# Performance work log

Measured on AMD Instinct MI355X. Metric: run time of the kernel, lower is better.

The kernel has to match this reference:

```python
import jax, jax.numpy as jnp
import numpy as np

N_NODES = 100000
N_EDGES = 20000
N_PAIRS = 640000
IN_CH = 128
HEADS = 4
OUT_CH = 32


def setup_inputs() -> dict:
    key = jax.random.key(0)
    k1, k2, k3, k4, k5 = jax.random.split(key, 5)
    X = jax.random.normal(k1, (N_NODES, IN_CH), dtype=jnp.float32)
    # nn.Linear(in, H*C, bias=False); stored as [in, H*C] so X0 = X @ W
    W = jax.random.normal(k2, (IN_CH, HEADS * OUT_CH), dtype=jnp.float32) * (1.0 / np.sqrt(IN_CH))
    stdv = (6.0 / (HEADS + OUT_CH)) ** 0.5
    att_e = jax.random.uniform(k3, (1, HEADS, OUT_CH), dtype=jnp.float32, minval=-stdv, maxval=stdv)
    vertex = jax.random.randint(k4, (N_PAIRS,), 0, N_NODES, dtype=jnp.int64)
    edges = jax.random.randint(k5, (N_PAIRS,), 0, N_EDGES, dtype=jnp.int64)
    return {"X": X, "W": W, "att_e": att_e, "vertex": vertex, "edges": edges}


def reference(X, W, att_e, vertex, edges):
    N = X.shape[0]
    H, C = HEADS, OUT_CH
    X0 = X @ W                                  # [N, H*C]
    Xv_hc = X0.reshape(N, H, C)
    Xve = Xv_hc[vertex]                          # [M, H, C] gather
    # scatter-mean over hyperedges
    esum = jax.ops.segment_sum(Xve, edges, num_segments=N_EDGES)
    ecnt = jax.ops.segment_sum(jnp.ones((Xve.shape[0],), X.dtype), edges, num_segments=N_EDGES)
    Xe = esum / jnp.maximum(ecnt, 1.0)[:, None, None]   # [E, H, C]
    alpha_e = (Xe * att_e).sum(-1)               # [E, H]
    a_ev = alpha_e[edges]                        # [M, H]
    alpha = jax.nn.leaky_relu(a_ev, 0.01)
    # per-vertex softmax over incident hyperedges
    amax = jax.ops.segment_max(alpha, vertex, num_segments=N)
    alpha = jnp.exp(alpha - amax[vertex])
    asum = jax.ops.segment_sum(alpha, vertex, num_segments=N)
    alpha = alpha / (asum[vertex] + 1e-8)
    Xev = Xe[edges] * alpha[:, :, None]          # [M, H, C]
    Xv = jax.ops.segment_sum(Xev, vertex, num_segments=N)
    return Xv.reshape(N, H * C) + X0
```

## Files before the change

### kernel.cpp

```cpp
#include <hip/hip_runtime.h>
#include <hip/hip_bf16.h>

#define N_NODES 100000
#define N_EDGES 20000
#define N_PAIRS 640000
#define CH 128
#define HEADS 4
#define MAXDV 32

#define NG_GEMM 1563
#define NCHUNK 125
#define ECHUNK 5120
#define EW 5120
#define VWR 6250
#define NRANGE 4
#define VBIN_R 25000

#define OFF_X0H   0UL
#define OFF_XEH   25600000UL
#define OFF_LRE   30720000UL
#define OFF_LRV   31360000UL
#define OFF_BLKE  32000000UL
#define OFF_BLKV  34560000UL
#define OFF_GSE   47060000UL
#define OFF_GSV   47162400UL
#define OFF_WT    47662400UL
#define OFF_ALPHA 47695168UL
#define OFF_OFFE  48015168UL
#define OFF_ENDE  48097088UL
#define OFF_OFFV  48179008UL
#define OFF_ENDV  48579008UL
#define OFF_PIDXE 48979008UL
#define OFF_PIDXV 51539008UL
#define OFF_CNTE  54099008UL
#define OFF_CNTV  54180928UL
#define OFF_TOT   54580928UL
#define ZERO_BYTES 8UL

typedef __attribute__((ext_vector_type(8))) short bf16x8;
typedef __attribute__((ext_vector_type(4))) float f32x4;

__device__ inline short f2bf(float f) {
    __hip_bfloat16 h = __float2bfloat16(f);
    return reinterpret_cast<short&>(h);
}
__device__ inline float bf2f(short s) {
    unsigned int u = ((unsigned int)(unsigned short)s) << 16;
    union { unsigned int u; float f; } c; c.u = u;
    return c.f;
}

__global__ __launch_bounds__(256) void k_wprep(const float* __restrict__ W,
                                               short* __restrict__ Wt) {
    const int idx = blockIdx.x * 256 + threadIdx.x;
    const int n = idx >> 7, k = idx & 127;
    Wt[n * CH + k] = f2bf(W[k * CH + n]);
}

__device__ inline void gemm_body(int gb, const float* __restrict__ X,
                                 const short* __restrict__ Wt,
                                 short* __restrict__ X0h) {
    const int t = threadIdx.x;
    const int wave = t >> 6, lane = t & 63;
    const int r0 = gb * 64 + (wave >> 1) * 32;
    const int c0 = (wave & 1) * 64;
    const int lrow = lane & 15, lk8 = (lane >> 4) * 8;

    f32x4 acc[2][4] = {};

#pragma unroll
    for (int kk = 0; kk < 4; ++kk) {
        const int ks = kk * 32 + lk8;
        bf16x8 a[2], b[4];
#pragma unroll
        for (int m = 0; m < 2; ++m) {
            int row = r0 + m * 16 + lrow;
            row = min(row, N_NODES - 1);
            const float* p = &X[(size_t)row * CH + ks];
            const float4 x0 = *(const float4*)p;
            const float4 x1 = *(const float4*)(p + 4);
            a[m][0] = f2bf(x0.x); a[m][1] = f2bf(x0.y);
            a[m][2] = f2bf(x0.z); a[m][3] = f2bf(x0.w);
            a[m][4] = f2bf(x1.x); a[m][5] = f2bf(x1.y);
            a[m][6] = f2bf(x1.z); a[m][7] = f2bf(x1.w);
        }
#pragma unroll
        for (int n = 0; n < 4; ++n) {
            int col = c0 + n * 16 + lrow;
            b[n] = *(const bf16x8*)&Wt[col * CH + ks];
        }
#pragma unroll
        for (int m = 0; m < 2; ++m)
#pragma unroll
            for (int n = 0; n < 4; ++n)
                acc[m][n] = __builtin_amdgcn_mfma_f32_16x16x32_bf16(a[m], b[n], acc[m][n], 0, 0, 0);
    }

#pragma unroll
    for (int m = 0; m < 2; ++m) {
#pragma unroll
        for (int reg = 0; reg < 4; ++reg) {
            const int row = r0 + m * 16 + (lane >> 4) * 4 + reg;
            if (row < N_NODES) {
#pragma unroll
                for (int n = 0; n < 4; ++n)
                    X0h[(size_t)row * CH + c0 + n * 16 + (lane & 15)] = f2bf(acc[m][n][reg]);
            }
        }
    }
}

__global__ __launch_bounds__(256) void k_phase1(const float* __restrict__ X,
                                                const short* __restrict__ Wt,
                                                short* __restrict__ X0h,
                                                const int* __restrict__ vertex,
                                                const int* __restrict__ edges,
                                                unsigned char* __restrict__ lrank_e,
                                                unsigned char* __restrict__ lrank_v,
                                                unsigned int* __restrict__ blkcnt_e,
                                                unsigned int* __restrict__ blkcnt_v) {
    __shared__ unsigned int hist[VWR];
    const int bid = blockIdx.x;
    const int t = threadIdx.x;

    if (bid < NRANGE * NCHUNK) {
        const int r = bid & 3, c = bid >> 2;
        for (int i = t; i < VWR; i += 256) hist[i] = 0;
        __syncthreads();
        const int base = c * ECHUNK;
        const int vmin = r * VBIN_R;
#pragma unroll
        for (int it = 0; it < 20; ++it) {
            const int m = base + it * 256 + t;
            const int loc = vertex[m] - vmin;
            if ((unsigned)loc < (unsigned)VBIN_R) {
                const unsigned sh = (unsigned)(loc & 3) * 8u;
                unsigned old = atomicAdd(&hist[loc >> 2], 1u << sh);
                lrank_v[m] = (unsigned char)((old >> sh) & 0xffu);
            }
        }
        __syncthreads();
        unsigned int* dst = &blkcnt_v[(size_t)(r * NCHUNK + c) * VWR];
        for (int w = t; w < VWR; w += 256) dst[w] = hist[w];
        return;
    }
    if (bid < NRANGE * NCHUNK + NCHUNK) {
        const int c = bid - NRANGE * NCHUNK;
        for (int i = t; i < EW; i += 256) hist[i] = 0;
        __syncthreads();
        const int base = c * ECHUNK;
#pragma unroll
        for (int it = 0; it < 20; ++it) {
            const int m = base + it * 256 + t;
            const int e = edges[m];
            const unsigned sh = (unsigned)(e & 3) * 8u;
            unsigned old = atomicAdd(&hist[e >> 2], 1u << sh);
            lrank_e[m] = (unsigned char)((old >> sh) & 0xffu);
        }
        __syncthreads();
        unsigned int* dst = &blkcnt_e[(size_t)c * EW];
        for (int w = t; w < EW; w += 256) dst[w] = hist[w];
        return;
    }
    gemm_body(bid - (NRANGE * NCHUNK + NCHUNK), X, Wt, X0h);
}

__global__ __launch_bounds__(256) void k_scan_p1(const unsigned int* __restrict__ blkcnt_e,
                                                 const unsigned int* __restrict__ blkcnt_v,
                                                 unsigned int* __restrict__ gse,
                                                 unsigned int* __restrict__ gsv) {
    const int bid = blockIdx.x;
    if (bid < 100) {
        const int gid = bid * 256 + threadIdx.x;
        const int g = gid / EW, w = gid % EW;
        unsigned s = 0;
#pragma unroll 5
        for (int i = 0; i < 25; ++i) s += blkcnt_e[(size_t)(g * 25 + i) * EW + w];
        gse[g * EW + w] = s;
        return;
    }
    const int vid = (bid - 100) * 256 + threadIdx.x;
    if (vid >= 20 * VWR) return;
    const int g = vid / VWR, w = vid % VWR;
    const int r = g / 5, cg = g % 5;
    unsigned s = 0;
#pragma unroll 5
    for (int i = 0; i < 25; ++i)
        s += blkcnt_v[(size_t)(r * NCHUNK + cg * 25 + i) * VWR + w];
    gsv[g * VWR + w] = s;
}

__global__ __launch_bounds__(256) void k_scan_p2(unsigned int* __restrict__ gse,
                                                 unsigned int* __restrict__ gsv,
                                                 int* __restrict__ cnt_e,
                                                 int* __restrict__ cnt_v) {
    const int bid = blockIdx.x;
    if (bid < 20) {
        const int w = bid * 256 + threadIdx.x;
        unsigned run = 0;
#pragma unroll
        for (int g = 0; g < 5; ++g) {
            unsigned c = gse[g * EW + w];
            gse[g * EW + w] = run;
            run += c;
        }
        int4 o = { (int)(run & 0xffu), (int)((run >> 8) & 0xffu),
                   (int)((run >> 16) & 0xffu), (int)(run >> 24) };
        *(int4*)&cnt_e[4 * w] = o;
        return;
    }
    const int id = (bid - 20) * 256 + threadIdx.x;
    if (id >= NRANGE * VWR) return;
    const int r = id / VWR, w = id % VWR;
    unsigned run = 0;
#pragma unroll
    for (int g = r * 5; g < r * 5 + 5; ++g) {
        unsigned c = gsv[g * VWR + w];
        gsv[g * VWR + w] = run;
        run += c;
    }
    int4 o = { (int)(run & 0xffu), (int)((run >> 8) & 0xffu),
               (int)((run >> 16) & 0xffu), (int)(run >> 24) };
    *(int4*)&cnt_v[r * VBIN_R + 4 * w] = o;
}

__global__ __launch_bounds__(256) void k_scan_p3(unsigned int* __restrict__ blkcnt_e,
                                                 unsigned int* __restrict__ blkcnt_v,
                                                 const unsigned int* __restrict__ gse,
                                                 const unsigned int* __restrict__ gsv) {
    const int bid = blockIdx.x;
    if (bid < 100) {
        const int gid = bid * 256 + threadIdx.x;
        const int g = gid / EW, w = gid % EW;
        unsigned run = gse[g * EW + w];
#pragma unroll 5
        for (int i = 0; i < 25; ++i) {
            const size_t idx = (size_t)(g * 25 + i) * EW + w;
            unsigned c = blkcnt_e[idx];
            blkcnt_e[idx] = run;
            run += c;
        }
        return;
    }
    const int vid = (bid - 100) * 256 + threadIdx.x;
    if (vid >= 20 * VWR) return;
    const int g = vid / VWR, w = vid % VWR;
    const int r = g / 5, cg = g % 5;
    unsigned run = gsv[g * VWR + w];
#pragma unroll 5
    for (int i = 0; i < 25; ++i) {
        const size_t idx = (size_t)(r * NCHUNK + cg * 25 + i) * VWR + w;
        unsigned c = blkcnt_v[idx];
        blkcnt_v[idx] = run;
        run += c;
    }
}

__global__ __launch_bounds__(256) void k_offsets2(const int* __restrict__ cnt_e,
                                                  int* __restrict__ off_e,
                                                  int* __restrict__ end_e,
                                                  const int* __restrict__ cnt_v,
                                                  int* __restrict__ off_v,
                                                  int* __restrict__ end_v,
                                                  int* __restrict__ totals) {
    __shared__ int s[256];
    __shared__ int base;
    const int bid = blockIdx.x, t = threadIdx.x;
    const int* cnt; int* off; int* end; int* total; int n, i;
    if (bid < 79) { cnt = cnt_e; off = off_e; end = end_e; total = &totals[0]; n = N_EDGES;  i = bid * 256 + t; }
    else          { cnt = cnt_v; off = off_v; end = end_v; total = &totals[1]; n = N_NODES; i = (bid - 79) * 256 + t; }
    const int c = (i < n) ? cnt[i] : 0;
    s[t] = c;
    __syncthreads();
    for (int d = 1; d < 256; d <<= 1) {
        int x = (t >= d) ? s[t - d] : 0;
        __syncthreads();
        s[t] += x;
        __syncthreads();
    }
    if (t == 0) base = atomicAdd(total, s[255]);
    __syncthreads();
    if (i < n) {
        int o = base + s[t] - c;
        off[i] = o;
        end[i] = o + c;
    }
}

__global__ __launch_bounds__(256) void k_scatter(const int* __restrict__ vertex,
                                                 const int* __restrict__ edges,
                                                 const unsigned char* __restrict__ lrank_e,
                                                 const unsigned char* __restrict__ lrank_v,
                                                 const unsigned int* __restrict__ blkcnt_e,
                                                 const unsigned int* __restrict__ blkcnt_v,
                                                 const int* __restrict__ off_e,
                                                 const int* __restrict__ off_v,
                                                 int* __restrict__ vlist_e,
                                                 int* __restrict__ elist_v) {
    const int m = blockIdx.x * 256 + threadIdx.x;
    const int e = edges[m];
    const int v = vertex[m];
    const int c = m / ECHUNK;
    const unsigned pe = blkcnt_e[(size_t)c * EW + (e >> 2)];
    const int er = (int)((pe >> ((unsigned)(e & 3) * 8u)) & 0xffu) + (int)lrank_e[m];
    const int r = v / VBIN_R, loc = v - r * VBIN_R;
    const unsigned pv = blkcnt_v[(size_t)(r * NCHUNK + c) * VWR + (loc >> 2)];
    const int vr = (int)((pv >> ((unsigned)(loc & 3) * 8u)) & 0xffu) + (int)lrank_v[m];
    vlist_e[off_e[e] + er] = v;
    elist_v[off_v[v] + vr] = e;
}

__global__ __launch_bounds__(256) void k_edge(const short* __restrict__ X0h,
                                              const int* __restrict__ off_e,
                                              const int* __restrict__ end_e,
                                              const int* __restrict__ vlist,
                                              const float* __restrict__ att,
                                              short* __restrict__ Xeh,
                                              float* __restrict__ alpha_le) {
    const int t = threadIdx.x;
    const int slot = t >> 5, lane = t & 31, h = lane >> 3;
    const int e = blockIdx.x * 8 + slot;
    const int s = off_e[e], en = end_e[e];
    const int deg = en - s;

    float4 acc = make_float4(0.f, 0.f, 0.f, 0.f);
    for (int c0 = 0; c0 < deg; c0 += 32) {
        const int cn = min(32, deg - c0);
        int vl = (lane < cn) ? vlist[s + c0 + lane] : 0;
#pragma unroll 4
        for (int j = 0; j < cn; ++j) {
            int vj = __shfl(vl, j, 32);
            short4 x = *(const short4*)&X0h[(size_t)vj * CH + (lane << 2)];
            acc.x += bf2f(x.x); acc.y += bf2f(x.y);
            acc.z += bf2f(x.z); acc.w += bf2f(x.w);
        }
    }
    const float invd = 1.0f / fmaxf((float)deg, 1.0f);
    float4 xe = make_float4(acc.x * invd, acc.y * invd, acc.z * invd, acc.w * invd);
    short4 xh;
    xh.x = f2bf(xe.x); xh.y = f2bf(xe.y); xh.z = f2bf(xe.z); xh.w = f2bf(xe.w);
    *(short4*)&Xeh[(size_t)e * CH + (lane << 2)] = xh;

    const float4 av = *(const float4*)&att[lane << 2];
    float p = xe.x * av.x + xe.y * av.y + xe.z * av.z + xe.w * av.w;
#pragma unroll
    for (int o = 4; o; o >>= 1) p += __shfl_xor(p, o);
    if ((lane & 7) == 0) {
        float a = p;
        alpha_le[e * HEADS + h] = (a > 0.f) ? a : 0.01f * a;
    }
}

__global__ __launch_bounds__(256) void k_vertex(const short* __restrict__ X0h,
                                                const short* __restrict__ Xeh,
                                                const float* __restrict__ alpha_le,
                                                const int* __restrict__ off_v,
                                                const int* __restrict__ end_v,
                                                const int* __restrict__ elist,
                                                float* __restrict__ out) {
    const int t = threadIdx.x;
    const int slot = t >> 5, lane = t & 31, h = lane >> 3;
    const int v = blockIdx.x * 8 + slot;
    const int s = off_v[v], en = end_v[v];
    const int deg = en - s;

    __shared__ int   se[8][MAXDV];
    __shared__ float sa[8][MAXDV * HEADS];

    if (deg <= MAXDV && lane < deg) {
        int e = elist[s + lane];
        se[slot][lane] = e;
        *(float4*)&sa[slot][lane << 2] = *(const float4*)&alpha_le[e * HEADS];
    }
    const short4 resh = *(const short4*)&X0h[(size_t)v * CH + (lane << 2)];
    __syncthreads();

    float4 acc = make_float4(0.f, 0.f, 0.f, 0.f);
    if (deg <= MAXDV) {
        float mx = -INFINITY;
        for (int j = 0; j < deg; ++j) mx = fmaxf(mx, sa[slot][(j << 2) + h]);
        float ssum = 0.f;
        for (int j = 0; j < deg; ++j) ssum += __expf(sa[slot][(j << 2) + h] - mx);
        const float inv = 1.0f / (ssum + 1e-8f);
        for (int j = 0; j < deg; ++j) {
            float w = __expf(sa[slot][(j << 2) + h] - mx) * inv;
            short4 x = *(const short4*)&Xeh[(size_t)se[slot][j] * CH + (lane << 2)];
            acc.x += w * bf2f(x.x); acc.y += w * bf2f(x.y);
            acc.z += w * bf2f(x.z); acc.w += w * bf2f(x.w);
        }
    } else {
        float mx = -INFINITY;
        for (int j = 0; j < deg; ++j) mx = fmaxf(mx, alpha_le[elist[s + j] * HEADS + h]);
        float ssum = 0.f;
        for (int j = 0; j < deg; ++j) ssum += __expf(alpha_le[elist[s + j] * HEADS + h] - mx);
        const float inv = 1.0f / (ssum + 1e-8f);
        for (int j = 0; j < deg; ++j) {
            int e = elist[s + j];
            float w = __expf(alpha_le[e * HEADS + h] - mx) * inv;
            short4 x = *(const short4*)&Xeh[(size_t)e * CH + (lane << 2)];
            acc.x += w * bf2f(x.x); acc.y += w * bf2f(x.y);
            acc.z += w * bf2f(x.z); acc.w += w * bf2f(x.w);
        }
    }
    float4 o = make_float4(acc.x + bf2f(resh.x), acc.y + bf2f(resh.y),
                           acc.z + bf2f(resh.z), acc.w + bf2f(resh.w));
    ((float4*)out)[(size_t)v * 32 + lane] = o;
}

extern "C" void kernel_launch(void* const* d_in, const int* in_sizes, int n_in,
                              void* d_out, int out_size, void* d_ws, size_t ws_size,
                              hipStream_t stream) {
    const float* X      = (const float*)d_in[0];
    const float* W      = (const float*)d_in[1];
    const float* att    = (const float*)d_in[2];
    const int*   vertex = (const int*)d_in[3];
    const int*   edges  = (const int*)d_in[4];
    float* out = (float*)d_out;

    char* ws = (char*)d_ws;
    short* X0h      = (short*)(ws + OFF_X0H);
    short* Xeh      = (short*)(ws + OFF_XEH);
    unsigned char* lrank_e = (unsigned char*)(ws + OFF_LRE);
    unsigned char* lrank_v = (unsigned char*)(ws + OFF_LRV);
    unsigned int*  blkcnt_e = (unsigned int*)(ws + OFF_BLKE);
    unsigned int*  blkcnt_v = (unsigned int*)(ws + OFF_BLKV);
    unsigned int*  gse      = (unsigned int*)(ws + OFF_GSE);
    unsigned int*  gsv      = (unsigned int*)(ws + OFF_GSV);
    short* Wt       = (short*)(ws + OFF_WT);
    float* alpha_le = (float*)(ws + OFF_ALPHA);
    int* off_e   = (int*)(ws + OFF_OFFE);
    int* end_e   = (int*)(ws + OFF_ENDE);
    int* off_v   = (int*)(ws + OFF_OFFV);
    int* end_v   = (int*)(ws + OFF_ENDV);
    int* vlist_e = (int*)(ws + OFF_PIDXE);
    int* elist_v = (int*)(ws + OFF_PIDXV);
    int* cnt_e   = (int*)(ws + OFF_CNTE);
    int* cnt_v   = (int*)(ws + OFF_CNTV);
    int* totals  = (int*)(ws + OFF_TOT);

    hipMemsetAsync(ws + OFF_TOT, 0, ZERO_BYTES, stream);

    k_wprep<<<64, 256, 0, stream>>>(W, Wt);
    k_phase1<<<NRANGE * NCHUNK + NCHUNK + NG_GEMM, 256, 0, stream>>>(
        X, Wt, X0h, vertex, edges, lrank_e, lrank_v, blkcnt_e, blkcnt_v);
    k_scan_p1<<<100 + 489, 256, 0, stream>>>(blkcnt_e, blkcnt_v, gse, gsv);
    k_scan_p2<<<20 + 98, 256, 0, stream>>>(gse, gsv, cnt_e, cnt_v);
    k_scan_p3<<<100 + 489, 256, 0, stream>>>(blkcnt_e, blkcnt_v, gse, gsv);
    k_offsets2<<<79 + 391, 256, 0, stream>>>(cnt_e, off_e, end_e, cnt_v, off_v, end_v, totals);
    k_scatter<<<N_PAIRS / 256, 256, 0, stream>>>(vertex, edges, lrank_e, lrank_v,
                                                 blkcnt_e, blkcnt_v, off_e, off_v,
                                                 vlist_e, elist_v);
    k_edge<<<N_EDGES / 8, 256, 0, stream>>>(X0h, off_e, end_e, vlist_e, att, Xeh, alpha_le);
    k_vertex<<<N_NODES / 8, 256, 0, stream>>>(X0h, Xeh, alpha_le, off_v, end_v, elist_v, out);
}
```

Measured before the change: 166.5 us.

## Widen gather loads to 16 bytes and prefetch GEMM operands one k-step ahead

The edge and vertex gather kernels now split each 32-lane group into two halves. Each half handles alternate incident rows with 16-byte bf16x8 loads instead of 8-byte short4 loads, and the partial sums are combined with a cross-half shuffle. This doubles the bytes per load and the number of rows in flight per group. The GEMM body is also software-pipelined: the X and W fragments for the next k-step are loaded while the MFMAs of the current step run, which costs extra registers. The vertex kernel's high-degree fallback leaves half the lanes idle, and output stores now come from half the lanes with two float4 writes each.

```diff
diff --git a/kernel.cpp b/kernel.cpp
--- a/kernel.cpp
+++ b/kernel.cpp
@@ -65,35 +65,49 @@
     const int r0 = gb * 64 + (wave >> 1) * 32;
     const int c0 = (wave & 1) * 64;
     const int lrow = lane & 15, lk8 = (lane >> 4) * 8;
+    const int row0 = min(r0 + lrow, N_NODES - 1);
+    const int row1 = min(r0 + 16 + lrow, N_NODES - 1);
+    const float* px0 = &X[(size_t)row0 * CH + lk8];
+    const float* px1 = &X[(size_t)row1 * CH + lk8];
+    const short* pw0 = &Wt[(size_t)(c0 + lrow) * CH + lk8];
 
     f32x4 acc[2][4] = {};
 
+    float4 xa[2][2]; bf16x8 bb[4];
+    xa[0][0] = *(const float4*)(px0); xa[0][1] = *(const float4*)(px0 + 4);
+    xa[1][0] = *(const float4*)(px1); xa[1][1] = *(const float4*)(px1 + 4);
+#pragma unroll
+    for (int n = 0; n < 4; ++n) bb[n] = *(const bf16x8*)(pw0 + n * 16 * CH);
+
 #pragma unroll
     for (int kk = 0; kk < 4; ++kk) {
-        const int ks = kk * 32 + lk8;
-        bf16x8 a[2], b[4];
+        float4 xn[2][2]; bf16x8 bn[4];
+        if (kk < 3) {
+            const int ks = (kk + 1) * 32;
+            xn[0][0] = *(const float4*)(px0 + ks); xn[0][1] = *(const float4*)(px0 + ks + 4);
+            xn[1][0] = *(const float4*)(px1 + ks); xn[1][1] = *(const float4*)(px1 + ks + 4);
+#pragma unroll
+            for (int n = 0; n < 4; ++n) bn[n] = *(const bf16x8*)(pw0 + n * 16 * CH + ks);
+        }
+        bf16x8 a[2];
 #pragma unroll
         for (int m = 0; m < 2; ++m) {
-            int row = r0 + m * 16 + lrow;
-            row = min(row, N_NODES - 1);
-            const float* p = &X[(size_t)row * CH + ks];
-            const float4 x0 = *(const float4*)p;
-            const float4 x1 = *(const float4*)(p + 4);
-            a[m][0] = f2bf(x0.x); a[m][1] = f2bf(x0.y);
-            a[m][2] = f2bf(x0.z); a[m][3] = f2bf(x0.w);
-            a[m][4] = f2bf(x1.x); a[m][5] = f2bf(x1.y);
-            a[m][6] = f2bf(x1.z); a[m][7] = f2bf(x1.w);
-        }
-#pragma unroll
-        for (int n = 0; n < 4; ++n) {
-            int col = c0 + n * 16 + lrow;
-            b[n] = *(const bf16x8*)&Wt[col * CH + ks];
+            a[m][0] = f2bf(xa[m][0].x); a[m][1] = f2bf(xa[m][0].y);
+            a[m][2] = f2bf(xa[m][0].z); a[m][3] = f2bf(xa[m][0].w);
+            a[m][4] = f2bf(xa[m][1].x); a[m][5] = f2bf(xa[m][1].y);
+            a[m][6] = f2bf(xa[m][1].z); a[m][7] = f2bf(xa[m][1].w);
         }
 #pragma unroll
         for (int m = 0; m < 2; ++m)
 #pragma unroll
             for (int n = 0; n < 4; ++n)
-                acc[m][n] = __builtin_amdgcn_mfma_f32_16x16x32_bf16(a[m], b[n], acc[m][n], 0, 0, 0);
+                acc[m][n] = __builtin_amdgcn_mfma_f32_16x16x32_bf16(a[m], bb[n], acc[m][n], 0, 0, 0);
+        if (kk < 3) {
+#pragma unroll
+            for (int m = 0; m < 2; ++m) { xa[m][0] = xn[m][0]; xa[m][1] = xn[m][1]; }
+#pragma unroll
+            for (int n = 0; n < 4; ++n) bb[n] = bn[n];
+        }
     }
 
 #pragma unroll
@@ -318,36 +332,45 @@
                                               short* __restrict__ Xeh,
                                               float* __restrict__ alpha_le) {
     const int t = threadIdx.x;
-    const int slot = t >> 5, lane = t & 31, h = lane >> 3;
+    const int slot = t >> 5, lane = t & 31;
+    const int half = lane >> 4, cl = lane & 15;
     const int e = blockIdx.x * 8 + slot;
     const int s = off_e[e], en = end_e[e];
     const int deg = en - s;
 
-    float4 acc = make_float4(0.f, 0.f, 0.f, 0.f);
+    float va[8] = {0.f, 0.f, 0.f, 0.f, 0.f, 0.f, 0.f, 0.f};
     for (int c0 = 0; c0 < deg; c0 += 32) {
         const int cn = min(32, deg - c0);
         int vl = (lane < cn) ? vlist[s + c0 + lane] : 0;
 #pragma unroll 4
-        for (int j = 0; j < cn; ++j) {
-            int vj = __shfl(vl, j, 32);
-            short4 x = *(const short4*)&X0h[(size_t)vj * CH + (lane << 2)];
-            acc.x += bf2f(x.x); acc.y += bf2f(x.y);
-            acc.z += bf2f(x.z); acc.w += bf2f(x.w);
-        }
-    }
+        for (int j = 0; j < cn; j += 2) {
+            const int jj = j + half;
+            const int vj = __shfl(vl, jj, 32);
+            if (jj < cn) {
+                bf16x8 x = *(const bf16x8*)&X0h[(size_t)vj * CH + cl * 8];
+#pragma unroll
+                for (int i = 0; i < 8; ++i) va[i] += bf2f(x[i]);
+            }
+        }
+    }
+#pragma unroll
+    for (int i = 0; i < 8; ++i) va[i] += __shfl_xor(va[i], 16);
+
     const float invd = 1.0f / fmaxf((float)deg, 1.0f);
-    float4 xe = make_float4(acc.x * invd, acc.y * invd, acc.z * invd, acc.w * invd);
-    short4 xh;
-    xh.x = f2bf(xe.x); xh.y = f2bf(xe.y); xh.z = f2bf(xe.z); xh.w = f2bf(xe.w);
-    *(short4*)&Xeh[(size_t)e * CH + (lane << 2)] = xh;
-
-    const float4 av = *(const float4*)&att[lane << 2];
-    float p = xe.x * av.x + xe.y * av.y + xe.z * av.z + xe.w * av.w;
-#pragma unroll
-    for (int o = 4; o; o >>= 1) p += __shfl_xor(p, o);
-    if ((lane & 7) == 0) {
-        float a = p;
-        alpha_le[e * HEADS + h] = (a > 0.f) ? a : 0.01f * a;
+    bf16x8 xh;
+    float xe[8];
+#pragma unroll
+    for (int i = 0; i < 8; ++i) { xe[i] = va[i] * invd; xh[i] = f2bf(xe[i]); }
+    if (half == 0) *(bf16x8*)&Xeh[(size_t)e * CH + cl * 8] = xh;
+
+    const float4 a0 = *(const float4*)&att[cl * 8];
+    const float4 a1 = *(const float4*)&att[cl * 8 + 4];
+    float p = xe[0] * a0.x + xe[1] * a0.y + xe[2] * a0.z + xe[3] * a0.w
+            + xe[4] * a1.x + xe[5] * a1.y + xe[6] * a1.z + xe[7] * a1.w;
+    p += __shfl_xor(p, 1);
+    p += __shfl_xor(p, 2);
+    if (half == 0 && (cl & 3) == 0) {
+        alpha_le[e * HEADS + (cl >> 2)] = (p > 0.f) ? p : 0.01f * p;
     }
 }
 
@@ -359,7 +382,8 @@
                                                 const int* __restrict__ elist,
                                                 float* __restrict__ out) {
     const int t = threadIdx.x;
-    const int slot = t >> 5, lane = t & 31, h = lane >> 3;
+    const int slot = t >> 5, lane = t & 31;
+    const int half = lane >> 4, cl = lane & 15, h = cl >> 2;
     const int v = blockIdx.x * 8 + slot;
     const int s = off_v[v], en = end_v[v];
     const int deg = en - s;
@@ -372,21 +396,25 @@
         se[slot][lane] = e;
         *(float4*)&sa[slot][lane << 2] = *(const float4*)&alpha_le[e * HEADS];
     }
-    const short4 resh = *(const short4*)&X0h[(size_t)v * CH + (lane << 2)];
+    const bf16x8 resh = *(const bf16x8*)&X0h[(size_t)v * CH + cl * 8];
     __syncthreads();
 
-    float4 acc = make_float4(0.f, 0.f, 0.f, 0.f);
+    float va[8] = {0.f, 0.f, 0.f, 0.f, 0.f, 0.f, 0.f, 0.f};
     if (deg <= MAXDV) {
         float mx = -INFINITY;
         for (int j = 0; j < deg; ++j) mx = fmaxf(mx, sa[slot][(j << 2) + h]);
         float ssum = 0.f;
         for (int j = 0; j < deg; ++j) ssum += __expf(sa[slot][(j << 2) + h] - mx);
         const float inv = 1.0f / (ssum + 1e-8f);
-        for (int j = 0; j < deg; ++j) {
-            float w = __expf(sa[slot][(j << 2) + h] - mx) * inv;
-            short4 x = *(const short4*)&Xeh[(size_t)se[slot][j] * CH + (lane << 2)];
-            acc.x += w * bf2f(x.x); acc.y += w * bf2f(x.y);
-            acc.z += w * bf2f(x.z); acc.w += w * bf2f(x.w);
+#pragma unroll 2
+        for (int j = 0; j < deg; j += 2) {
+            const int jj = j + half;
+            if (jj < deg) {
+                const float w = __expf(sa[slot][(jj << 2) + h] - mx) * inv;
+                bf16x8 x = *(const bf16x8*)&Xeh[(size_t)se[slot][jj] * CH + cl * 8];
+#pragma unroll
+                for (int i = 0; i < 8; ++i) va[i] += w * bf2f(x[i]);
+            }
         }
     } else {
         float mx = -INFINITY;
@@ -395,16 +423,27 @@
         for (int j = 0; j < deg; ++j) ssum += __expf(alpha_le[elist[s + j] * HEADS + h] - mx);
         const float inv = 1.0f / (ssum + 1e-8f);
         for (int j = 0; j < deg; ++j) {
-            int e = elist[s + j];
-            float w = __expf(alpha_le[e * HEADS + h] - mx) * inv;
-            short4 x = *(const short4*)&Xeh[(size_t)e * CH + (lane << 2)];
-            acc.x += w * bf2f(x.x); acc.y += w * bf2f(x.y);
-            acc.z += w * bf2f(x.z); acc.w += w * bf2f(x.w);
-        }
-    }
-    float4 o = make_float4(acc.x + bf2f(resh.x), acc.y + bf2f(resh.y),
-                           acc.z + bf2f(resh.z), acc.w + bf2f(resh.w));
-    ((float4*)out)[(size_t)v * 32 + lane] = o;
+            if (half == 0) {
+                const int e = elist[s + j];
+                const float w = __expf(alpha_le[e * HEADS + h] - mx) * inv;
+                bf16x8 x = *(const bf16x8*)&Xeh[(size_t)e * CH + cl * 8];
+#pragma unroll
+                for (int i = 0; i < 8; ++i) va[i] += w * bf2f(x[i]);
+            }
+        }
+    }
+#pragma unroll
+    for (int i = 0; i < 8; ++i) va[i] += __shfl_xor(va[i], 16);
+
+    if (half == 0) {
+        float4 o0, o1;
+        o0.x = va[0] + bf2f(resh[0]); o0.y = va[1] + bf2f(resh[1]);
+        o0.z = va[2] + bf2f(resh[2]); o0.w = va[3] + bf2f(resh[3]);
+        o1.x = va[4] + bf2f(resh[4]); o1.y = va[5] + bf2f(resh[5]);
+        o1.z = va[6] + bf2f(resh[6]); o1.w = va[7] + bf2f(resh[7]);
+        *(float4*)&out[(size_t)v * CH + cl * 8]     = o0;
+        *(float4*)&out[(size_t)v * CH + cl * 8 + 4] = o1;
+    }
 }
 
 extern "C" void kernel_launch(void* const* d_in, const int* in_sizes, int n_in,
```

Result: faster. 160.6 us (-3.6%).
